# Optimization experiments

Measured on AMD Instinct MI355X. Metric: run time of the kernel, lower is better.

Reference implementation:

```python
import jax, jax.numpy as jnp
import numpy as np

N_HEAD = 16


def setup_inputs() -> dict:
    key = jax.random.key(0)
    ks = jax.random.split(key, 6)
    B, S, D = 2, 2048, 1024
    w = 0.02
    return {
        "x": jax.random.normal(ks[0], (B, S, D), dtype=jnp.float32),
        "attention_mask": jnp.ones((B, S), dtype=jnp.int32),
        "Wq": jax.random.normal(ks[1], (D, D), dtype=jnp.float32) * w,
        "bq": jnp.zeros((D,), dtype=jnp.float32),
        "Wk": jax.random.normal(ks[2], (D, D), dtype=jnp.float32) * w,
        "bk": jnp.zeros((D,), dtype=jnp.float32),
        "Wv": jax.random.normal(ks[3], (D, D), dtype=jnp.float32) * w,
        "bv": jnp.zeros((D,), dtype=jnp.float32),
        "Wp": jax.random.normal(ks[4], (D, D), dtype=jnp.float32) * w,
        "bp": jnp.zeros((D,), dtype=jnp.float32),
    }


def reference(x, attention_mask, Wq, bq, Wk, bk, Wv, bv, Wp, bp):
    # x: (B,S,D); PyTorch Linear: y = x @ W.T + b
    B, S, D = x.shape
    H = N_HEAD
    HD = D // H
    scale = 1.0 / jnp.sqrt(jnp.asarray(HD, dtype=x.dtype))

    def heads(W, b):
        return (x @ W.T + b).reshape(B, S, H, HD).transpose(0, 2, 1, 3)  # (B,H,S,HD)

    q = heads(Wq, bq)
    k = heads(Wk, bk)
    v = heads(Wv, bv)

    logits = jnp.einsum("bhsd,bhtd->bhst", q, k) * scale  # (B,H,S,S)

    causal = jnp.tril(jnp.ones((S, S), dtype=bool))  # (S,S)
    am = attention_mask.astype(bool)
    mask = causal[None, None, :, :] & (am[:, None, :, None] & am[:, None, None, :])

    float_min = jnp.finfo(x.dtype).min
    logits = jnp.where(mask, logits, float_min)
    w = jax.nn.softmax(logits, axis=-1)  # dropout is identity in eval / p=0

    attn = jnp.einsum("bhst,bhtd->bhsd", w, v)  # (B,H,S,HD)
    attn = attn.transpose(0, 2, 1, 3).reshape(B, S, D)
    return attn @ Wp.T + bp
```

## Files before the change

### kernel.cpp

```cpp
#include <hip/hip_runtime.h>


#define BB 2
#define SS 2048
#define DD 1024
#define HH 16
#define HDD 64
#define NEG_BIG (-1.0e30f)
#define QSCL 0.18033688011112042f

typedef __attribute__((ext_vector_type(8))) short short8;
typedef __attribute__((ext_vector_type(4))) float floatx4;
typedef unsigned int u32;
#define AS_GLOBAL __attribute__((address_space(1)))
#define AS_LDS    __attribute__((address_space(3)))

__device__ __forceinline__ ushort f2bf(float f) {
    unsigned u = __float_as_uint(f);
    u += 0x7fffu + ((u >> 16) & 1u);
    return (ushort)(u >> 16);
}
__device__ __forceinline__ unsigned pk2(float a, float b) {
    return ((unsigned)f2bf(b) << 16) | (unsigned)f2bf(a);
}
__device__ __forceinline__ unsigned cvtpk(float a, float b) {
    unsigned r;
    asm("v_cvt_pk_bf16_f32 %0, %1, %2" : "=v"(r) : "v"(a), "v"(b));
    return r;
}
__device__ __forceinline__ void unpack8(const uint4 u, float* d) {
    d[0] = __uint_as_float(u.x << 16);
    d[1] = __uint_as_float(u.x & 0xffff0000u);
    d[2] = __uint_as_float(u.y << 16);
    d[3] = __uint_as_float(u.y & 0xffff0000u);
    d[4] = __uint_as_float(u.z << 16);
    d[5] = __uint_as_float(u.z & 0xffff0000u);
    d[6] = __uint_as_float(u.w << 16);
    d[7] = __uint_as_float(u.w & 0xffff0000u);
}
__device__ __forceinline__ void dma16(void* lds, const void* g) {
    __builtin_amdgcn_global_load_lds((const AS_GLOBAL u32*)g, (AS_LDS u32*)lds,
                                     16, 0, 0);
}

__global__ __launch_bounds__(256) void cvt_all(
    const float* __restrict__ x, const float* __restrict__ wq,
    const float* __restrict__ wk, const float* __restrict__ wv,
    const float* __restrict__ wp,
    ushort* __restrict__ dst, ushort* __restrict__ wp_dst)
{
    const size_t flat = ((size_t)blockIdx.x * 256 + threadIdx.x) * 8;
    const float* s;
    ushort* d = dst + flat;
    size_t off;
    float scl = 1.0f;
    if (flat < (size_t)4194304)      { s = x;  off = flat; }
    else if (flat < (size_t)5242880) { s = wq; off = flat - 4194304; scl = QSCL; }
    else if (flat < (size_t)6291456) { s = wk; off = flat - 5242880; }
    else if (flat < (size_t)7340032) { s = wv; off = flat - 6291456; }
    else { s = wp; off = flat - 7340032; d = wp_dst + off; }
    const float4 a = ((const float4*)(s + off))[0];
    const float4 b = ((const float4*)(s + off))[1];
    uint4 u;
    u.x = pk2(a.x * scl, a.y * scl); u.y = pk2(a.z * scl, a.w * scl);
    u.z = pk2(b.x * scl, b.y * scl); u.w = pk2(b.z * scl, b.w * scl);
    *(uint4*)d = u;
}

__global__ __launch_bounds__(256) void gemm_qkv_wa(
    const ushort* __restrict__ A,
    const ushort* __restrict__ W0, const ushort* __restrict__ W1,
    const ushort* __restrict__ W2,
    const float* __restrict__ B0, const float* __restrict__ B1,
    const float* __restrict__ B2,
    ushort* __restrict__ O0, ushort* __restrict__ O1, ushort* __restrict__ O2)
{
    __shared__ ushort As[128 * 32];
    __shared__ ushort Bs[128 * 32];
    __shared__ float bias_s[128];

    const int z = blockIdx.z;
    const ushort* W = (z == 0) ? W0 : (z == 1 ? W1 : W2);
    const float* bias = (z == 0) ? B0 : (z == 1 ? B1 : B2);
    ushort* out = (z == 0) ? O0 : (z == 1 ? O1 : O2);
    const bool isv = (z == 2);

    const int tid = threadIdx.x;
    const int bm = blockIdx.x * 128, bn = blockIdx.y * 128;
    const int wave = tid >> 6, lane = tid & 63, quad = lane >> 4, lm = lane & 15;
    const int r0 = tid >> 2, c0 = (tid & 3) * 8;
    const int c0g = ((tid & 3) ^ ((tid >> 3) & 3)) * 8;
    const int csw8 = (quad ^ ((lm >> 1) & 3)) * 8;

    if (tid < 128) {
        float bb = bias[bn + tid];
        if (z == 0) bb *= QSCL;
        bias_s[tid] = bb;
    }

    const floatx4 zz = {0.f, 0.f, 0.f, 0.f};
    floatx4 acc[16];
#pragma unroll
    for (int i = 0; i < 16; ++i) acc[i] = zz;

    const ushort* a0 = A + (size_t)(bm + r0) * DD + c0g;
    const ushort* a1 = A + (size_t)(bm + 64 + r0) * DD + c0g;
    const ushort* w0 = W + (size_t)(bn + r0) * DD + c0g;
    const ushort* w1 = W + (size_t)(bn + 64 + r0) * DD + c0g;
    ushort* const lA0 = &As[r0 * 32 + c0];
    ushort* const lA1 = &As[(64 + r0) * 32 + c0];
    ushort* const lB0 = &Bs[r0 * 32 + c0];
    ushort* const lB1 = &Bs[(64 + r0) * 32 + c0];

    for (int k0 = 0; k0 < DD; k0 += 32) {
        __syncthreads();
        dma16(lA0, a0); dma16(lA1, a1);
        dma16(lB0, w0); dma16(lB1, w1);
        a0 += 32; a1 += 32; w0 += 32; w1 += 32;
        __syncthreads();

        if (isv) {
            const short8 bf0 = *(const short8*)&Bs[(wave * 32 + lm) * 32 + csw8];
            const short8 bf1 = *(const short8*)&Bs[(wave * 32 + 16 + lm) * 32 + csw8];
#pragma unroll
            for (int i = 0; i < 8; ++i) {
                const short8 af = *(const short8*)&As[(i * 16 + lm) * 32 + csw8];
                acc[i * 2 + 0] = __builtin_amdgcn_mfma_f32_16x16x32_bf16(
                    af, bf0, acc[i * 2 + 0], 0, 0, 0);
                acc[i * 2 + 1] = __builtin_amdgcn_mfma_f32_16x16x32_bf16(
                    af, bf1, acc[i * 2 + 1], 0, 0, 0);
            }
        } else {
            const short8 af0 = *(const short8*)&As[(wave * 32 + lm) * 32 + csw8];
            const short8 af1 = *(const short8*)&As[(wave * 32 + 16 + lm) * 32 + csw8];
#pragma unroll
            for (int j = 0; j < 8; ++j) {
                const short8 bf = *(const short8*)&Bs[(j * 16 + lm) * 32 + csw8];
                acc[j] = __builtin_amdgcn_mfma_f32_16x16x32_bf16(
                    bf, af0, acc[j], 0, 0, 0);
                acc[8 + j] = __builtin_amdgcn_mfma_f32_16x16x32_bf16(
                    bf, af1, acc[8 + j], 0, 0, 0);
            }
        }
    }

    if (isv) {
        const int b = bm >> 11, sbase = bm & 2047;
#pragma unroll
        for (int j = 0; j < 2; ++j) {
            const int n = bn + wave * 32 + j * 16 + lm;
            const float bb = bias_s[n - bn];
            ushort* orow = out + ((size_t)(b * DD + n)) * SS;
#pragma unroll
            for (int i = 0; i < 8; ++i) {
                const floatx4 a = acc[i * 2 + j];
                ushort4 v;
                v.x = f2bf(a[0] + bb); v.y = f2bf(a[1] + bb);
                v.z = f2bf(a[2] + bb); v.w = f2bf(a[3] + bb);
                *(ushort4*)(orow + sbase + i * 16 + quad * 4) = v;
            }
        }
    } else {
#pragma unroll
        for (int i = 0; i < 2; ++i) {
            const int m = bm + wave * 32 + i * 16 + lm;
            const int b = m >> 11, s = m & 2047;
#pragma unroll
            for (int j = 0; j < 8; ++j) {
                const int nl = j * 16 + quad * 4;
                const int n = bn + nl;
                const int h = n >> 6, hd = n & 63;
                const floatx4 a = acc[i * 8 + j];
                ushort4 v;
                v.x = f2bf(a[0] + bias_s[nl + 0]);
                v.y = f2bf(a[1] + bias_s[nl + 1]);
                v.z = f2bf(a[2] + bias_s[nl + 2]);
                v.w = f2bf(a[3] + bias_s[nl + 3]);
                *(ushort4*)(out + (((size_t)(b * HH + h) * SS) + s) * HDD + hd) = v;
            }
        }
    }
}

__global__ __launch_bounds__(256, 2) void gemm_proj_rs(
    const ushort* __restrict__ A, const ushort* __restrict__ W,
    const float* __restrict__ bias, float* __restrict__ out)
{
    __shared__ ushort As[128 * 32];
    __shared__ ushort Bs[128 * 32];
    __shared__ float bias_s[128];

    const int tid = threadIdx.x;
    const int bm = blockIdx.x * 128, bn = blockIdx.y * 128;
    const int wave = tid >> 6, lane = tid & 63, quad = lane >> 4, lm = lane & 15;
    const int wm = wave >> 1, wn = wave & 1;
    const int r0 = tid >> 2, c0 = (tid & 3) * 8;
    const int c0s = ((tid & 3) ^ ((tid >> 3) & 3)) * 8;
    const int csw8 = (quad ^ ((lm >> 1) & 3)) * 8;

    if (tid < 128) bias_s[tid] = bias[bn + tid];

    const floatx4 zz = {0.f, 0.f, 0.f, 0.f};
    floatx4 acc[4][4];
#pragma unroll
    for (int i = 0; i < 4; ++i)
#pragma unroll
        for (int j = 0; j < 4; ++j) acc[i][j] = zz;

    const ushort* ap = A + (size_t)(bm + r0) * DD + c0;
    const ushort* wpp = W + (size_t)(bn + r0) * DD + c0;

    uint4 ar0, ar1, wr0, wr1;
#define LOADT(K0)                                                \
    do {                                                         \
        ar0 = *(const uint4*)(ap + (K0));                        \
        ar1 = *(const uint4*)(ap + (size_t)64 * DD + (K0));      \
        wr0 = *(const uint4*)(wpp + (K0));                       \
        wr1 = *(const uint4*)(wpp + (size_t)64 * DD + (K0));     \
    } while (0)
#define STORET()                                                 \
    do {                                                         \
        *(uint4*)&As[r0 * 32 + c0s] = ar0;                       \
        *(uint4*)&As[(64 + r0) * 32 + c0s] = ar1;                \
        *(uint4*)&Bs[r0 * 32 + c0s] = wr0;                       \
        *(uint4*)&Bs[(64 + r0) * 32 + c0s] = wr1;                \
    } while (0)

    LOADT(0);
    STORET();
    __syncthreads();

    for (int k0 = 0; k0 < DD; k0 += 32) {
        const bool have_nxt = (k0 + 32) < DD;
        if (have_nxt) LOADT(k0 + 32);

        short8 af[4], bf[4];
#pragma unroll
        for (int i = 0; i < 4; ++i)
            af[i] = *(const short8*)&As[(wm * 64 + i * 16 + lm) * 32 + csw8];
#pragma unroll
        for (int j = 0; j < 4; ++j)
            bf[j] = *(const short8*)&Bs[(wn * 64 + j * 16 + lm) * 32 + csw8];
#pragma unroll
        for (int i = 0; i < 4; ++i)
#pragma unroll
            for (int j = 0; j < 4; ++j)
                acc[i][j] = __builtin_amdgcn_mfma_f32_16x16x32_bf16(
                    bf[j], af[i], acc[i][j], 0, 0, 0);

        if (have_nxt) {
            __syncthreads();
            STORET();
            __syncthreads();
        }
    }
#undef LOADT
#undef STORET

#pragma unroll
    for (int i = 0; i < 4; ++i) {
#pragma unroll
        for (int j = 0; j < 4; ++j) {
            const int nl = wn * 64 + j * 16 + quad * 4;
            const int n = bn + nl;
            const int m = bm + wm * 64 + i * 16 + lm;
            float4 v;
            v.x = acc[i][j][0] + bias_s[nl + 0];
            v.y = acc[i][j][1] + bias_s[nl + 1];
            v.z = acc[i][j][2] + bias_s[nl + 2];
            v.w = acc[i][j][3] + bias_s[nl + 3];
            *(float4*)(out + (size_t)m * DD + n) = v;
        }
    }
}

__global__ __launch_bounds__(256) void attn_mfma(
    const ushort* __restrict__ Q, const ushort* __restrict__ K,
    const ushort* __restrict__ Vt, const int* __restrict__ am,
    ushort* __restrict__ Opart, float* __restrict__ lbuf)
{
    __shared__ ushort Ks[64 * 72];
    __shared__ ushort Vts[64 * 72];
    __shared__ ushort Ps[4][32 * 72];
    __shared__ int amk_s[64];

    const int tid = threadIdx.x;
    const int wq = tid >> 6, lane = tid & 63, quad = lane >> 4, lm = lane & 15;
    const int bh = blockIdx.y, b = bh >> 4, h = bh & 15;
    const int qt = b ? (int)blockIdx.x : (int)(gridDim.x - 1 - blockIdx.x);
    const int split = blockIdx.z;
    const size_t base = (size_t)bh * SS * HDD;
    const size_t tbase = (size_t)bh * HDD * SS;
    const int* amrow = am + b * SS;
    const int q0 = qt * 128 + wq * 32;

    short8 qf[2][2];
#pragma unroll
    for (int sub = 0; sub < 2; ++sub) {
        const ushort* qp = Q + base + (size_t)(q0 + sub * 16 + lm) * HDD + quad * 8;
        qf[sub][0] = *(const short8*)qp;
        qf[sub][1] = *(const short8*)(qp + 32);
    }
    int amq[2];
#pragma unroll
    for (int sub = 0; sub < 2; ++sub) amq[sub] = amrow[q0 + sub * 16 + lm];
    const bool allq = __all(amq[0] != 0 && amq[1] != 0);

    const floatx4 zz = {0.f, 0.f, 0.f, 0.f};
    floatx4 o_acc[2][4];
#pragma unroll
    for (int sub = 0; sub < 2; ++sub)
#pragma unroll
        for (int n2 = 0; n2 < 4; ++n2) o_acc[sub][n2] = zz;
    float l_lane[2] = {0.f, 0.f};

    const int sr = tid >> 2, sc = (tid & 3) * 16;
    const int ktmax = 2 * qt + 1;

    uint4 kra, krb, vra, vrb;
    int amr = 1;
    {
        const ushort* kp = K + base + (size_t)(split * 64 + sr) * HDD + sc;
        kra = ((const uint4*)kp)[0]; krb = ((const uint4*)kp)[1];
        const ushort* vp = Vt + tbase + (size_t)sr * SS + split * 64 + sc;
        vra = ((const uint4*)vp)[0]; vrb = ((const uint4*)vp)[1];
        if (tid < 64) amr = amrow[split * 64 + tid];
    }
    *(uint4*)&Ks[sr * 72 + sc] = kra;
    *(uint4*)&Ks[sr * 72 + sc + 8] = krb;
    *(uint4*)&Vts[sr * 72 + sc] = vra;
    *(uint4*)&Vts[sr * 72 + sc + 8] = vrb;
    if (tid < 64) amk_s[tid] = amr;
    __syncthreads();

    for (int kt = split; kt <= ktmax; kt += 2) {
        const int nxt = kt + 2;
        const bool have_nxt = nxt <= ktmax;
        if (have_nxt) {
            const ushort* kp = K + base + (size_t)(nxt * 64 + sr) * HDD + sc;
            kra = ((const uint4*)kp)[0]; krb = ((const uint4*)kp)[1];
            const ushort* vp = Vt + tbase + (size_t)sr * SS + nxt * 64 + sc;
            vra = ((const uint4*)vp)[0]; vrb = ((const uint4*)vp)[1];
            if (tid < 64) amr = amrow[nxt * 64 + tid];
        }

        const bool allk = (__ballot(amk_s[lane] != 0) == ~0ull);
        const bool fast = allk & allq & ((kt * 64 + 63) <= q0);
        if (fast) {
#pragma unroll
            for (int nt = 0; nt < 4; ++nt) {
                const short8 kf0 = *(const short8*)&Ks[(nt * 16 + lm) * 72 + quad * 8];
                const short8 kf1 = *(const short8*)&Ks[(nt * 16 + lm) * 72 + 32 + quad * 8];
#pragma unroll
                for (int sub = 0; sub < 2; ++sub) {
                    floatx4 s = zz;
                    s = __builtin_amdgcn_mfma_f32_16x16x32_bf16(kf0, qf[sub][0], s, 0, 0, 0);
                    s = __builtin_amdgcn_mfma_f32_16x16x32_bf16(kf1, qf[sub][1], s, 0, 0, 0);
                    const float e0 = exp2f(fminf(s[0], 40.f));
                    const float e1 = exp2f(fminf(s[1], 40.f));
                    const float e2 = exp2f(fminf(s[2], 40.f));
                    const float e3 = exp2f(fminf(s[3], 40.f));
                    l_lane[sub] += (e0 + e1) + (e2 + e3);
                    uint2 pv;
                    pv.x = cvtpk(e0, e1); pv.y = cvtpk(e2, e3);
                    *(uint2*)&Ps[wq][(sub * 16 + lm) * 72 + nt * 16 + quad * 4] = pv;
                }
            }
        } else {
#pragma unroll
            for (int nt = 0; nt < 4; ++nt) {
                const short8 kf0 = *(const short8*)&Ks[(nt * 16 + lm) * 72 + quad * 8];
                const short8 kf1 = *(const short8*)&Ks[(nt * 16 + lm) * 72 + 32 + quad * 8];
                const int4 amk4 = *(const int4*)&amk_s[nt * 16 + quad * 4];
#pragma unroll
                for (int sub = 0; sub < 2; ++sub) {
                    floatx4 s = zz;
                    s = __builtin_amdgcn_mfma_f32_16x16x32_bf16(kf0, qf[sub][0], s, 0, 0, 0);
                    s = __builtin_amdgcn_mfma_f32_16x16x32_bf16(kf1, qf[sub][1], s, 0, 0, 0);
                    const int qg = q0 + sub * 16 + lm;
                    const int t0 = kt * 64 + nt * 16 + quad * 4;
                    const bool mq = amq[sub] != 0;
                    const bool ok0 = amk4.x && mq && (t0 + 0 <= qg);
                    const bool ok1 = amk4.y && mq && (t0 + 1 <= qg);
                    const bool ok2 = amk4.z && mq && (t0 + 2 <= qg);
                    const bool ok3 = amk4.w && mq && (t0 + 3 <= qg);
                    const float e0 = exp2f(fminf(ok0 ? s[0] : NEG_BIG, 40.f));
                    const float e1 = exp2f(fminf(ok1 ? s[1] : NEG_BIG, 40.f));
                    const float e2 = exp2f(fminf(ok2 ? s[2] : NEG_BIG, 40.f));
                    const float e3 = exp2f(fminf(ok3 ? s[3] : NEG_BIG, 40.f));
                    l_lane[sub] += (e0 + e1) + (e2 + e3);
                    uint2 pv;
                    pv.x = cvtpk(e0, e1); pv.y = cvtpk(e2, e3);
                    *(uint2*)&Ps[wq][(sub * 16 + lm) * 72 + nt * 16 + quad * 4] = pv;
                }
            }
        }

        short8 af[2][2];
#pragma unroll
        for (int sub = 0; sub < 2; ++sub) {
            af[sub][0] = *(const short8*)&Ps[wq][(sub * 16 + lm) * 72 + quad * 8];
            af[sub][1] = *(const short8*)&Ps[wq][(sub * 16 + lm) * 72 + 32 + quad * 8];
        }
#pragma unroll
        for (int n2 = 0; n2 < 4; ++n2) {
            const short8 vf0 = *(const short8*)&Vts[(n2 * 16 + lm) * 72 + quad * 8];
            const short8 vf1 = *(const short8*)&Vts[(n2 * 16 + lm) * 72 + 32 + quad * 8];
#pragma unroll
            for (int sub = 0; sub < 2; ++sub) {
                o_acc[sub][n2] = __builtin_amdgcn_mfma_f32_16x16x32_bf16(
                    vf0, af[sub][0], o_acc[sub][n2], 0, 0, 0);
                o_acc[sub][n2] = __builtin_amdgcn_mfma_f32_16x16x32_bf16(
                    vf1, af[sub][1], o_acc[sub][n2], 0, 0, 0);
            }
        }

        if (have_nxt) {
            __syncthreads();
            *(uint4*)&Ks[sr * 72 + sc] = kra;
            *(uint4*)&Ks[sr * 72 + sc + 8] = krb;
            *(uint4*)&Vts[sr * 72 + sc] = vra;
            *(uint4*)&Vts[sr * 72 + sc + 8] = vrb;
            if (tid < 64) amk_s[tid] = amr;
            __syncthreads();
        }
    }

#pragma unroll
    for (int sub = 0; sub < 2; ++sub) {
        float l = l_lane[sub];
        l += __shfl_xor(l, 16);
        l += __shfl_xor(l, 32);
        if (quad == 0)
            lbuf[(size_t)split * (BB * HH * SS) + (size_t)bh * SS + q0 + sub * 16 + lm] = l;
        const int srow = q0 + sub * 16 + lm;
#pragma unroll
        for (int n2 = 0; n2 < 4; ++n2) {
            uint2 v;
            v.x = cvtpk(o_acc[sub][n2][0], o_acc[sub][n2][1]);
            v.y = cvtpk(o_acc[sub][n2][2], o_acc[sub][n2][3]);
            *(uint2*)(Opart + (size_t)split * (BB * SS * DD)
                        + ((size_t)(b * SS + srow)) * DD + h * HDD + n2 * 16 + quad * 4) = v;
        }
    }
}

__global__ __launch_bounds__(256) void combine(
    const ushort* __restrict__ Opart, const float* __restrict__ lbuf,
    ushort* __restrict__ Aout)
{
    const size_t e = ((size_t)blockIdx.x * 256 + threadIdx.x) * 8;
    const int m = (int)(e >> 10);
    const int col = (int)(e & 1023);
    const int b = m >> 11, s = m & 2047, h = col >> 6;
    const float l = lbuf[(b * HH + h) * SS + s]
                  + lbuf[BB * HH * SS + (b * HH + h) * SS + s];
    const float inv = l > 0.f ? 1.f / l : 0.f;
    const uint4 u0 = *(const uint4*)(Opart + e);
    const uint4 u1 = *(const uint4*)(Opart + (size_t)BB * SS * DD + e);
    float f0[8], f1[8];
    unpack8(u0, f0);
    unpack8(u1, f1);
    uint4 o;
    o.x = pk2((f0[0] + f1[0]) * inv, (f0[1] + f1[1]) * inv);
    o.y = pk2((f0[2] + f1[2]) * inv, (f0[3] + f1[3]) * inv);
    o.z = pk2((f0[4] + f1[4]) * inv, (f0[5] + f1[5]) * inv);
    o.w = pk2((f0[6] + f1[6]) * inv, (f0[7] + f1[7]) * inv);
    *(uint4*)(Aout + e) = o;
}

extern "C" void kernel_launch(void* const* d_in, const int* in_sizes, int n_in,
                              void* d_out, int out_size, void* d_ws, size_t ws_size,
                              hipStream_t stream) {
    const float* x  = (const float*)d_in[0];
    const int*   am = (const int*)d_in[1];
    const float* Wq = (const float*)d_in[2];
    const float* bq = (const float*)d_in[3];
    const float* Wk = (const float*)d_in[4];
    const float* bk = (const float*)d_in[5];
    const float* Wv = (const float*)d_in[6];
    const float* bv = (const float*)d_in[7];
    const float* Wp = (const float*)d_in[8];
    const float* bp = (const float*)d_in[9];
    float* out = (float*)d_out;

    const size_t elems = (size_t)BB * HH * SS * HDD;
    ushort* q_ws = (ushort*)d_ws;
    ushort* k_ws = q_ws + elems;
    ushort* v_ws = k_ws + elems;
    float*  lbuf = (float*)(v_ws + elems);
    ushort* wpb  = (ushort*)(lbuf + 2 * BB * HH * SS);

    ushort* xb  = (ushort*)d_out;
    ushort* wqb = xb + 4194304;
    ushort* wkb = wqb + 1048576;
    ushort* wvb = wkb + 1048576;

    cvt_all<<<4096, 256, 0, stream>>>(x, Wq, Wk, Wv, Wp, xb, wpb);

    gemm_qkv_wa<<<dim3(32, 8, 3), 256, 0, stream>>>(
        xb, wqb, wkb, wvb, bq, bk, bv, q_ws, k_ws, v_ws);

    attn_mfma<<<dim3(SS / 128, BB * HH, 2), 256, 0, stream>>>(
        q_ws, k_ws, v_ws, am, (ushort*)d_out, lbuf);

    combine<<<2048, 256, 0, stream>>>((const ushort*)d_out, lbuf, q_ws);

    gemm_proj_rs<<<dim3(32, 8), 256, 0, stream>>>(q_ws, wpb, bp, out);
}
```

Measured before the change: 218.1 us.

## Pair complementary 64-row query tiles per block for causal load balance

Each attention block now handles 64-row query tiles, with one wave per 16 rows, and processes two tiles in sequence: tile p and tile 31-p. This gives every block the same total amount of causal key work. It replaces the earlier 128-row tiles with a reversed ordering for one batch. Each wave now holds a single 16-row query fragment, which lowers register and LDS use, but the K/V tiles are reloaded for the second phase and per-wave MFMA work per K tile is halved.

```diff
diff --git a/kernel.cpp b/kernel.cpp
--- a/kernel.cpp
+++ b/kernel.cpp
@@ -281,166 +281,152 @@
 {
     __shared__ ushort Ks[64 * 72];
     __shared__ ushort Vts[64 * 72];
-    __shared__ ushort Ps[4][32 * 72];
+    __shared__ ushort Ps[4][16 * 72];
     __shared__ int amk_s[64];
 
     const int tid = threadIdx.x;
     const int wq = tid >> 6, lane = tid & 63, quad = lane >> 4, lm = lane & 15;
     const int bh = blockIdx.y, b = bh >> 4, h = bh & 15;
-    const int qt = b ? (int)blockIdx.x : (int)(gridDim.x - 1 - blockIdx.x);
-    const int split = blockIdx.z;
+    const int pslot = (int)blockIdx.x;
+    const int split = (int)blockIdx.z;
     const size_t base = (size_t)bh * SS * HDD;
     const size_t tbase = (size_t)bh * HDD * SS;
     const int* amrow = am + b * SS;
-    const int q0 = qt * 128 + wq * 32;
-
-    short8 qf[2][2];
-#pragma unroll
-    for (int sub = 0; sub < 2; ++sub) {
-        const ushort* qp = Q + base + (size_t)(q0 + sub * 16 + lm) * HDD + quad * 8;
-        qf[sub][0] = *(const short8*)qp;
-        qf[sub][1] = *(const short8*)(qp + 32);
-    }
-    int amq[2];
-#pragma unroll
-    for (int sub = 0; sub < 2; ++sub) amq[sub] = amrow[q0 + sub * 16 + lm];
-    const bool allq = __all(amq[0] != 0 && amq[1] != 0);
-
+    const int sr = tid >> 2, sc = (tid & 3) * 16;
     const floatx4 zz = {0.f, 0.f, 0.f, 0.f};
-    floatx4 o_acc[2][4];
-#pragma unroll
-    for (int sub = 0; sub < 2; ++sub)
-#pragma unroll
-        for (int n2 = 0; n2 < 4; ++n2) o_acc[sub][n2] = zz;
-    float l_lane[2] = {0.f, 0.f};
-
-    const int sr = tid >> 2, sc = (tid & 3) * 16;
-    const int ktmax = 2 * qt + 1;
-
-    uint4 kra, krb, vra, vrb;
-    int amr = 1;
-    {
-        const ushort* kp = K + base + (size_t)(split * 64 + sr) * HDD + sc;
-        kra = ((const uint4*)kp)[0]; krb = ((const uint4*)kp)[1];
-        const ushort* vp = Vt + tbase + (size_t)sr * SS + split * 64 + sc;
-        vra = ((const uint4*)vp)[0]; vrb = ((const uint4*)vp)[1];
-        if (tid < 64) amr = amrow[split * 64 + tid];
-    }
-    *(uint4*)&Ks[sr * 72 + sc] = kra;
-    *(uint4*)&Ks[sr * 72 + sc + 8] = krb;
-    *(uint4*)&Vts[sr * 72 + sc] = vra;
-    *(uint4*)&Vts[sr * 72 + sc + 8] = vrb;
-    if (tid < 64) amk_s[tid] = amr;
-    __syncthreads();
-
-    for (int kt = split; kt <= ktmax; kt += 2) {
-        const int nxt = kt + 2;
-        const bool have_nxt = nxt <= ktmax;
-        if (have_nxt) {
-            const ushort* kp = K + base + (size_t)(nxt * 64 + sr) * HDD + sc;
-            kra = ((const uint4*)kp)[0]; krb = ((const uint4*)kp)[1];
-            const ushort* vp = Vt + tbase + (size_t)sr * SS + nxt * 64 + sc;
-            vra = ((const uint4*)vp)[0]; vrb = ((const uint4*)vp)[1];
-            if (tid < 64) amr = amrow[nxt * 64 + tid];
-        }
-
-        const bool allk = (__ballot(amk_s[lane] != 0) == ~0ull);
-        const bool fast = allk & allq & ((kt * 64 + 63) <= q0);
-        if (fast) {
-#pragma unroll
-            for (int nt = 0; nt < 4; ++nt) {
-                const short8 kf0 = *(const short8*)&Ks[(nt * 16 + lm) * 72 + quad * 8];
-                const short8 kf1 = *(const short8*)&Ks[(nt * 16 + lm) * 72 + 32 + quad * 8];
-#pragma unroll
-                for (int sub = 0; sub < 2; ++sub) {
-                    floatx4 s = zz;
-                    s = __builtin_amdgcn_mfma_f32_16x16x32_bf16(kf0, qf[sub][0], s, 0, 0, 0);
-                    s = __builtin_amdgcn_mfma_f32_16x16x32_bf16(kf1, qf[sub][1], s, 0, 0, 0);
-                    const float e0 = exp2f(fminf(s[0], 40.f));
-                    const float e1 = exp2f(fminf(s[1], 40.f));
-                    const float e2 = exp2f(fminf(s[2], 40.f));
-                    const float e3 = exp2f(fminf(s[3], 40.f));
-                    l_lane[sub] += (e0 + e1) + (e2 + e3);
-                    uint2 pv;
-                    pv.x = cvtpk(e0, e1); pv.y = cvtpk(e2, e3);
-                    *(uint2*)&Ps[wq][(sub * 16 + lm) * 72 + nt * 16 + quad * 4] = pv;
-                }
-            }
-        } else {
-#pragma unroll
-            for (int nt = 0; nt < 4; ++nt) {
-                const short8 kf0 = *(const short8*)&Ks[(nt * 16 + lm) * 72 + quad * 8];
-                const short8 kf1 = *(const short8*)&Ks[(nt * 16 + lm) * 72 + 32 + quad * 8];
-                const int4 amk4 = *(const int4*)&amk_s[nt * 16 + quad * 4];
-#pragma unroll
-                for (int sub = 0; sub < 2; ++sub) {
-                    floatx4 s = zz;
-                    s = __builtin_amdgcn_mfma_f32_16x16x32_bf16(kf0, qf[sub][0], s, 0, 0, 0);
-                    s = __builtin_amdgcn_mfma_f32_16x16x32_bf16(kf1, qf[sub][1], s, 0, 0, 0);
-                    const int qg = q0 + sub * 16 + lm;
-                    const int t0 = kt * 64 + nt * 16 + quad * 4;
-                    const bool mq = amq[sub] != 0;
-                    const bool ok0 = amk4.x && mq && (t0 + 0 <= qg);
-                    const bool ok1 = amk4.y && mq && (t0 + 1 <= qg);
-                    const bool ok2 = amk4.z && mq && (t0 + 2 <= qg);
-                    const bool ok3 = amk4.w && mq && (t0 + 3 <= qg);
-                    const float e0 = exp2f(fminf(ok0 ? s[0] : NEG_BIG, 40.f));
-                    const float e1 = exp2f(fminf(ok1 ? s[1] : NEG_BIG, 40.f));
-                    const float e2 = exp2f(fminf(ok2 ? s[2] : NEG_BIG, 40.f));
-                    const float e3 = exp2f(fminf(ok3 ? s[3] : NEG_BIG, 40.f));
-                    l_lane[sub] += (e0 + e1) + (e2 + e3);
-                    uint2 pv;
-                    pv.x = cvtpk(e0, e1); pv.y = cvtpk(e2, e3);
-                    *(uint2*)&Ps[wq][(sub * 16 + lm) * 72 + nt * 16 + quad * 4] = pv;
-                }
-            }
-        }
-
-        short8 af[2][2];
-#pragma unroll
-        for (int sub = 0; sub < 2; ++sub) {
-            af[sub][0] = *(const short8*)&Ps[wq][(sub * 16 + lm) * 72 + quad * 8];
-            af[sub][1] = *(const short8*)&Ps[wq][(sub * 16 + lm) * 72 + 32 + quad * 8];
-        }
-#pragma unroll
-        for (int n2 = 0; n2 < 4; ++n2) {
-            const short8 vf0 = *(const short8*)&Vts[(n2 * 16 + lm) * 72 + quad * 8];
-            const short8 vf1 = *(const short8*)&Vts[(n2 * 16 + lm) * 72 + 32 + quad * 8];
-#pragma unroll
-            for (int sub = 0; sub < 2; ++sub) {
-                o_acc[sub][n2] = __builtin_amdgcn_mfma_f32_16x16x32_bf16(
-                    vf0, af[sub][0], o_acc[sub][n2], 0, 0, 0);
-                o_acc[sub][n2] = __builtin_amdgcn_mfma_f32_16x16x32_bf16(
-                    vf1, af[sub][1], o_acc[sub][n2], 0, 0, 0);
-            }
-        }
-
-        if (have_nxt) {
-            __syncthreads();
+
+#pragma unroll
+    for (int ph = 0; ph < 2; ++ph) {
+        const int qt64 = ph ? (31 - pslot) : pslot;
+        const int q0 = qt64 * 64;
+        const int ktend = qt64;
+        const int qrow = q0 + wq * 16 + lm;
+
+        if (ph) __syncthreads();
+
+        short8 qf0, qf1;
+        {
+            const ushort* qp = Q + base + (size_t)qrow * HDD + quad * 8;
+            qf0 = *(const short8*)qp;
+            qf1 = *(const short8*)(qp + 32);
+        }
+        const int amq = amrow[qrow];
+        const bool allq = __all(amq != 0);
+
+        floatx4 o_acc[4];
+#pragma unroll
+        for (int n2 = 0; n2 < 4; ++n2) o_acc[n2] = zz;
+        float l_lane = 0.f;
+
+        if (split <= ktend) {
+            uint4 kra, krb, vra, vrb;
+            int amr = 1;
+            {
+                const ushort* kp = K + base + (size_t)(split * 64 + sr) * HDD + sc;
+                kra = ((const uint4*)kp)[0]; krb = ((const uint4*)kp)[1];
+                const ushort* vp = Vt + tbase + (size_t)sr * SS + split * 64 + sc;
+                vra = ((const uint4*)vp)[0]; vrb = ((const uint4*)vp)[1];
+                if (tid < 64) amr = amrow[split * 64 + tid];
+            }
             *(uint4*)&Ks[sr * 72 + sc] = kra;
             *(uint4*)&Ks[sr * 72 + sc + 8] = krb;
             *(uint4*)&Vts[sr * 72 + sc] = vra;
             *(uint4*)&Vts[sr * 72 + sc + 8] = vrb;
             if (tid < 64) amk_s[tid] = amr;
             __syncthreads();
-        }
-    }
-
-#pragma unroll
-    for (int sub = 0; sub < 2; ++sub) {
-        float l = l_lane[sub];
+
+            for (int kt = split; kt <= ktend; kt += 2) {
+                const int nxt = kt + 2;
+                const bool have_nxt = nxt <= ktend;
+                if (have_nxt) {
+                    const ushort* kp = K + base + (size_t)(nxt * 64 + sr) * HDD + sc;
+                    kra = ((const uint4*)kp)[0]; krb = ((const uint4*)kp)[1];
+                    const ushort* vp = Vt + tbase + (size_t)sr * SS + nxt * 64 + sc;
+                    vra = ((const uint4*)vp)[0]; vrb = ((const uint4*)vp)[1];
+                    if (tid < 64) amr = amrow[nxt * 64 + tid];
+                }
+
+                const bool allk = (__ballot(amk_s[lane] != 0) == ~0ull);
+                const bool fast = allk & allq & ((kt * 64 + 63) <= (q0 + wq * 16));
+                if (fast) {
+#pragma unroll
+                    for (int nt = 0; nt < 4; ++nt) {
+                        const short8 kf0 = *(const short8*)&Ks[(nt * 16 + lm) * 72 + quad * 8];
+                        const short8 kf1 = *(const short8*)&Ks[(nt * 16 + lm) * 72 + 32 + quad * 8];
+                        floatx4 s = zz;
+                        s = __builtin_amdgcn_mfma_f32_16x16x32_bf16(kf0, qf0, s, 0, 0, 0);
+                        s = __builtin_amdgcn_mfma_f32_16x16x32_bf16(kf1, qf1, s, 0, 0, 0);
+                        const float e0 = exp2f(fminf(s[0], 40.f));
+                        const float e1 = exp2f(fminf(s[1], 40.f));
+                        const float e2 = exp2f(fminf(s[2], 40.f));
+                        const float e3 = exp2f(fminf(s[3], 40.f));
+                        l_lane += (e0 + e1) + (e2 + e3);
+                        uint2 pv;
+                        pv.x = cvtpk(e0, e1); pv.y = cvtpk(e2, e3);
+                        *(uint2*)&Ps[wq][lm * 72 + nt * 16 + quad * 4] = pv;
+                    }
+                } else {
+#pragma unroll
+                    for (int nt = 0; nt < 4; ++nt) {
+                        const short8 kf0 = *(const short8*)&Ks[(nt * 16 + lm) * 72 + quad * 8];
+                        const short8 kf1 = *(const short8*)&Ks[(nt * 16 + lm) * 72 + 32 + quad * 8];
+                        const int4 amk4 = *(const int4*)&amk_s[nt * 16 + quad * 4];
+                        floatx4 s = zz;
+                        s = __builtin_amdgcn_mfma_f32_16x16x32_bf16(kf0, qf0, s, 0, 0, 0);
+                        s = __builtin_amdgcn_mfma_f32_16x16x32_bf16(kf1, qf1, s, 0, 0, 0);
+                        const int t0 = kt * 64 + nt * 16 + quad * 4;
+                        const bool mq = amq != 0;
+                        const bool ok0 = amk4.x && mq && (t0 + 0 <= qrow);
+                        const bool ok1 = amk4.y && mq && (t0 + 1 <= qrow);
+                        const bool ok2 = amk4.z && mq && (t0 + 2 <= qrow);
+                        const bool ok3 = amk4.w && mq && (t0 + 3 <= qrow);
+                        const float e0 = exp2f(fminf(ok0 ? s[0] : NEG_BIG, 40.f));
+                        const float e1 = exp2f(fminf(ok1 ? s[1] : NEG_BIG, 40.f));
+                        const float e2 = exp2f(fminf(ok2 ? s[2] : NEG_BIG, 40.f));
+                        const float e3 = exp2f(fminf(ok3 ? s[3] : NEG_BIG, 40.f));
+                        l_lane += (e0 + e1) + (e2 + e3);
+                        uint2 pv;
+                        pv.x = cvtpk(e0, e1); pv.y = cvtpk(e2, e3);
+                        *(uint2*)&Ps[wq][lm * 72 + nt * 16 + quad * 4] = pv;
+                    }
+                }
+
+                const short8 af0 = *(const short8*)&Ps[wq][lm * 72 + quad * 8];
+                const short8 af1 = *(const short8*)&Ps[wq][lm * 72 + 32 + quad * 8];
+#pragma unroll
+                for (int n2 = 0; n2 < 4; ++n2) {
+                    const short8 vf0 = *(const short8*)&Vts[(n2 * 16 + lm) * 72 + quad * 8];
+                    const short8 vf1 = *(const short8*)&Vts[(n2 * 16 + lm) * 72 + 32 + quad * 8];
+                    o_acc[n2] = __builtin_amdgcn_mfma_f32_16x16x32_bf16(
+                        vf0, af0, o_acc[n2], 0, 0, 0);
+                    o_acc[n2] = __builtin_amdgcn_mfma_f32_16x16x32_bf16(
+                        vf1, af1, o_acc[n2], 0, 0, 0);
+                }
+
+                if (have_nxt) {
+                    __syncthreads();
+                    *(uint4*)&Ks[sr * 72 + sc] = kra;
+                    *(uint4*)&Ks[sr * 72 + sc + 8] = krb;
+                    *(uint4*)&Vts[sr * 72 + sc] = vra;
+                    *(uint4*)&Vts[sr * 72 + sc + 8] = vrb;
+                    if (tid < 64) amk_s[tid] = amr;
+                    __syncthreads();
+                }
+            }
+        }
+
+        float l = l_lane;
         l += __shfl_xor(l, 16);
         l += __shfl_xor(l, 32);
         if (quad == 0)
-            lbuf[(size_t)split * (BB * HH * SS) + (size_t)bh * SS + q0 + sub * 16 + lm] = l;
-        const int srow = q0 + sub * 16 + lm;
+            lbuf[(size_t)split * (BB * HH * SS) + (size_t)bh * SS + qrow] = l;
 #pragma unroll
         for (int n2 = 0; n2 < 4; ++n2) {
             uint2 v;
-            v.x = cvtpk(o_acc[sub][n2][0], o_acc[sub][n2][1]);
-            v.y = cvtpk(o_acc[sub][n2][2], o_acc[sub][n2][3]);
+            v.x = cvtpk(o_acc[n2][0], o_acc[n2][1]);
+            v.y = cvtpk(o_acc[n2][2], o_acc[n2][3]);
             *(uint2*)(Opart + (size_t)split * (BB * SS * DD)
-                        + ((size_t)(b * SS + srow)) * DD + h * HDD + n2 * 16 + quad * 4) = v;
+                        + ((size_t)(b * SS + qrow)) * DD + h * HDD + n2 * 16 + quad * 4) = v;
         }
     }
 }
@@ -501,7 +487,7 @@
     gemm_qkv_wa<<<dim3(32, 8, 3), 256, 0, stream>>>(
         xb, wqb, wkb, wvb, bq, bk, bv, q_ws, k_ws, v_ws);
 
-    attn_mfma<<<dim3(SS / 128, BB * HH, 2), 256, 0, stream>>>(
+    attn_mfma<<<dim3(16, BB * HH, 2), 256, 0, stream>>>(
         q_ws, k_ws, v_ws, am, (ushort*)d_out, lbuf);
 
     combine<<<2048, 256, 0, stream>>>((const ushort*)d_out, lbuf, q_ws);
```

New measurement: 216.0 us. About the same (-1.0%).
